# Performance work log

Hardware: AMD Instinct MI355X
Metric: run time of the kernel (lower is better)

The kernel has to match this reference:

```python
import jax, jax.numpy as jnp
import numpy as np

B_IN, C, K, P, STRIDE, ITERS = 32, 32, 3, 4, 2, 3
PSIZE = P * P


def _patch(t):
    # t: (b, h, w, B, d) -> (b, oh, ow, K, K, B, d), matching torch fancy-index patching
    b, h, w = t.shape[:3]
    oh = int((h - K + 1) / STRIDE)
    idx = (np.arange(oh) * STRIDE)[:, None] + np.arange(K)[None, :]  # (oh, K)
    t = t[:, idx]          # (b, oh, K, w, B, d)
    t = t[:, :, :, idx]    # (b, oh, K, ow, K, B, d)
    perm = (0, 1, 3, 2, 4) + tuple(range(5, t.ndim))
    return jnp.transpose(t, perm), oh, oh


def _forward(x, a, weights, beta_u, beta_a):
    b = x.shape[0]
    KKB = K * K * B_IN
    p_in, oh, ow = _patch(x)
    a_in, _, _ = _patch(a)
    pose = p_in.reshape(b, oh, ow, KKB, P, P)
    a_in = a_in.reshape(b, oh, ow, KKB, 1)
    # voting: per-capsule 4x4 matmul with transformation matrices
    v = jnp.einsum('bhwnij,ncjl->bhwncil', pose, weights).reshape(b, oh, ow, KKB, C, PSIZE)
    eps = 1e-6
    lam = 1e-3
    ln2pi = np.float32(np.log(2.0 * np.pi))
    mu = sigma_sq = a_out = None
    for it in range(ITERS):
        if it == 0:
            r = jnp.full((b, oh, ow, KKB, C), 1.0 / C, jnp.float32) * a_in  # a_in broadcasts over C
        else:
            # gaussian log-likelihood of each vote under each output capsule
            ln_pjh = -(v - mu) ** 2 / (2.0 * sigma_sq) - 0.5 * jnp.log(sigma_sq) - 0.5 * ln2pi
            ln_ap = ln_pjh.sum(axis=5) + jnp.log(a_out.reshape(b, oh, ow, 1, C))
            r = jax.nn.softmax(ln_ap, axis=4)
        r_sum = r.sum(axis=3, keepdims=True)               # (b,oh,ow,1,C)
        coeff = (r / (r_sum + eps))[..., None]             # (b,oh,ow,KKB,C,1)
        mu = (coeff * v).sum(axis=3, keepdims=True)        # (b,oh,ow,1,C,PSIZE)
        sigma_sq = (coeff * (v - mu) ** 2).sum(axis=3, keepdims=True) + eps
        # beta_u: (C,1) broadcasts against (...,C,PSIZE); log(sqrt(s)) == 0.5*log(s)
        cost_h = (beta_u + 0.5 * jnp.log(sigma_sq)) * r_sum[..., None]
        a_out = jax.nn.sigmoid(lam * (beta_a - cost_h.sum(axis=5, keepdims=True)))
    p_out = mu.reshape(b, oh, ow, C, PSIZE)
    a_out = a_out.reshape(b, oh, ow, C, 1)
    return p_out, a_out


def setup_inputs() -> dict:
    key = jax.random.key(0)
    k1, k2, k3, k4, k5 = jax.random.split(key, 5)
    x = jax.random.normal(k1, (8, 14, 14, B_IN, PSIZE), jnp.float32)
    a = jax.random.uniform(k2, (8, 14, 14, B_IN, 1), jnp.float32)
    weights = jax.random.normal(k3, (K * K * B_IN, C, P, P), jnp.float32)
    beta_u = jax.random.normal(k4, (C, 1), jnp.float32) * 0.1
    beta_a = jax.random.normal(k5, (C, 1), jnp.float32) * 0.1
    return {"x": x, "a": a, "weights": weights, "beta_u": beta_u, "beta_a": beta_a}


def reference(x, a, weights, beta_u, beta_a):
    return _forward(x, a, weights, beta_u, beta_a)
```

## Files before the change

kernel.cpp:

```cpp
#include <hip/hip_runtime.h>

#define APB 256
#define NPOS 288
#define NCH 6
#define CHUNK 48
#define PSTRIDE 1056


template<int IT>
__global__ __launch_bounds__(APB) void caps_acc(
    const float* __restrict__ xg,
    const float* __restrict__ ag,
    const float* __restrict__ wg,
    const float* __restrict__ bu,
    const float* __restrict__ ba,
    const float* __restrict__ pin,
    float* __restrict__ pout)
{
    __shared__ __align__(16) float pose_s[CHUNK * 16];
    __shared__ float a_s[CHUNK];
    __shared__ __align__(16) float scratch[4 * 32 * 33];
    __shared__ float rsum_part[4 * 32];
    __shared__ float mu_tab[512];
    __shared__ float i2s_tab[512];
    __shared__ float Kc_tab[32];

    const int tid = threadIdx.x;
    const int blk = blockIdx.x;
    const int pos = blk / NCH;
    const int ch  = blk - pos * NCH;
    const int bb  = pos / 36;
    const int rem = pos % 36;
    const int yy  = rem / 6;
    const int xx  = rem % 6;

    #pragma unroll
    for (int j = 0; j < 3; ++j) {
        const int e    = ch * 768 + j * 256 + tid;
        const int cell = e >> 9;
        const int off  = e & 511;
        const int kh = cell / 3, kw = cell % 3;
        pose_s[j * 256 + tid] =
            xg[(size_t)((((bb * 14) + (2 * yy + kh)) * 14 + (2 * xx + kw)) * 32) * 16 + off];
    }
    if (IT == 0) {
        if (tid < CHUNK) {
            const int e    = ch * CHUNK + tid;
            const int cell = e >> 5;
            const int bi   = e & 31;
            const int kh = cell / 3, kw = cell % 3;
            a_s[tid] = ag[(size_t)(((bb * 14) + (2 * yy + kh)) * 14 + (2 * xx + kw)) * 32 + bi];
        }
    }

    const int fc2 = tid >> 3;
    const int fh  = tid & 7;
    if (IT > 0) {
        const float* q0 = pin + (size_t)pos * (NCH * PSTRIDE) + fc2 * 33;
        float ms0 = 0.f, ms1 = 0.f, vs0 = 0.f, vs1 = 0.f, rsc = 0.f;
        #pragma unroll
        for (int cc = 0; cc < NCH; ++cc) {
            const float* q = q0 + cc * PSTRIDE;
            ms0 += q[fh];
            ms1 += q[fh + 8];
            vs0 += q[16 + fh];
            vs1 += q[16 + fh + 8];
            rsc += q[32];
        }
        const float inv  = 1.f / (rsc + 1e-6f);
        const float S    = rsc * inv;
        const float mu0  = ms0 * inv;
        const float mu1  = ms1 * inv;
        const float sig0 = vs0 * inv - mu0 * mu0 * (2.f - S) + 1e-6f;
        const float sig1 = vs1 * inv - mu1 * mu1 * (2.f - S) + 1e-6f;
        float lgs = __logf(sig0) + __logf(sig1);
        #pragma unroll
        for (int msk = 4; msk >= 1; msk >>= 1) lgs += __shfl_xor(lgs, msk);
        const float cost = rsc * (16.f * bu[fc2] + 0.5f * lgs);
        const float ao   = 1.f / (1.f + __expf(-0.001f * (ba[fc2] - cost)));
        mu_tab[fc2 * 16 + fh]      = mu0;
        mu_tab[fc2 * 16 + fh + 8]  = mu1;
        i2s_tab[fc2 * 16 + fh]     = 0.5f / sig0;
        i2s_tab[fc2 * 16 + fh + 8] = 0.5f / sig1;
        if (fh == 0) Kc_tab[fc2] = 0.5f * lgs - __logf(ao);
    }
    __syncthreads();

    const int c    = tid & 31;
    const int s    = tid >> 5;
    const int lane = tid & 63;
    const int wv   = tid >> 6;
    const float4* wp = (const float4*)wg;

    float mu_c[16], i2s_c[16], Kc = 0.f;
    if (IT > 0) {
        #pragma unroll
        for (int p = 0; p < 16; ++p) {
            mu_c[p]  = mu_tab[c * 16 + p];
            i2s_c[p] = i2s_tab[c * 16 + p];
        }
        Kc = Kc_tab[c];
    }
    float macc[16], vacc[16], rs = 0.f;
    #pragma unroll
    for (int p = 0; p < 16; ++p) { macc[p] = 0.f; vacc[p] = 0.f; }

    for (int k = 0; k < 6; ++k) {
        const int nl = s * 6 + k;
        const int n  = ch * CHUNK + nl;
        const float4* pp = (const float4*)&pose_s[nl << 4];
        float pf[16];
        float4 q;
        q = pp[0]; pf[0]=q.x;  pf[1]=q.y;  pf[2]=q.z;  pf[3]=q.w;
        q = pp[1]; pf[4]=q.x;  pf[5]=q.y;  pf[6]=q.z;  pf[7]=q.w;
        q = pp[2]; pf[8]=q.x;  pf[9]=q.y;  pf[10]=q.z; pf[11]=q.w;
        q = pp[3]; pf[12]=q.x; pf[13]=q.y; pf[14]=q.z; pf[15]=q.w;
        const int wbase = (n * 32 + c) * 4;
        float v[16];
        #pragma unroll
        for (int p = 0; p < 16; ++p) v[p] = 0.f;
        #pragma unroll
        for (int j = 0; j < 4; ++j) {
            const float4 w = wp[wbase + j];
            #pragma unroll
            for (int i = 0; i < 4; ++i) {
                const float pj = pf[i * 4 + j];
                v[i*4+0] = fmaf(pj, w.x, v[i*4+0]);
                v[i*4+1] = fmaf(pj, w.y, v[i*4+1]);
                v[i*4+2] = fmaf(pj, w.z, v[i*4+2]);
                v[i*4+3] = fmaf(pj, w.w, v[i*4+3]);
            }
        }
        float r;
        if (IT == 0) {
            r = a_s[nl] * 0.03125f;
        } else {
            float t0 = 0.f, t1 = 0.f, t2 = 0.f, t3 = 0.f;
            #pragma unroll
            for (int p = 0; p < 16; p += 4) {
                float d0 = v[p]   - mu_c[p];   t0 = fmaf(d0*d0, i2s_c[p],   t0);
                float d1 = v[p+1] - mu_c[p+1]; t1 = fmaf(d1*d1, i2s_c[p+1], t1);
                float d2 = v[p+2] - mu_c[p+2]; t2 = fmaf(d2*d2, i2s_c[p+2], t2);
                float d3 = v[p+3] - mu_c[p+3]; t3 = fmaf(d3*d3, i2s_c[p+3], t3);
            }
            float lnap = -((t0 + t1) + (t2 + t3)) - Kc;
            float m = lnap;
            #pragma unroll
            for (int msk = 16; msk >= 1; msk >>= 1) m = fmaxf(m, __shfl_xor(m, msk));
            float e = __expf(lnap - m);
            float sum = e;
            #pragma unroll
            for (int msk = 16; msk >= 1; msk >>= 1) sum += __shfl_xor(sum, msk);
            r = e / sum;
        }
        rs += r;
        #pragma unroll
        for (int p = 0; p < 16; ++p) {
            float rv = r * v[p];
            macc[p] += rv;
            vacc[p] = fmaf(rv, v[p], vacc[p]);
        }
    }

    #pragma unroll
    for (int p = 0; p < 16; ++p) {
        macc[p] += __shfl_xor(macc[p], 32);
        vacc[p] += __shfl_xor(vacc[p], 32);
    }
    rs += __shfl_xor(rs, 32);
    if (lane < 32) {
        const int base = (wv * 32 + lane) * 33;
        #pragma unroll
        for (int p = 0; p < 16; ++p) {
            scratch[base + p]      = macc[p];
            scratch[base + 16 + p] = vacc[p];
        }
        rsum_part[wv * 32 + lane] = rs;
    }
    __syncthreads();

    float ms0 = 0.f, ms1 = 0.f, vs0 = 0.f, vs1 = 0.f, rsc = 0.f;
    #pragma unroll
    for (int w = 0; w < 4; ++w) {
        const int base = (w * 32 + fc2) * 33;
        ms0 += scratch[base + fh];
        ms1 += scratch[base + fh + 8];
        vs0 += scratch[base + 16 + fh];
        vs1 += scratch[base + 16 + fh + 8];
        rsc += rsum_part[w * 32 + fc2];
    }
    float* po = pout + (size_t)(pos * NCH + ch) * PSTRIDE + fc2 * 33;
    po[fh]          = ms0;
    po[fh + 8]      = ms1;
    po[16 + fh]     = vs0;
    po[16 + fh + 8] = vs1;
    if (fh == 0) po[32] = rsc;
}

__global__ __launch_bounds__(512) void caps_fin(
    const float* __restrict__ pin,
    const float* __restrict__ bu,
    const float* __restrict__ ba,
    float* __restrict__ outp)
{
    const int tid = threadIdx.x;
    const int pos = blockIdx.x;
    const int fc = tid >> 4, fp = tid & 15;
    const float* q0 = pin + (size_t)pos * (NCH * PSTRIDE) + fc * 33;
    float ms = 0.f, vs = 0.f, rsc = 0.f;
    #pragma unroll
    for (int cc = 0; cc < NCH; ++cc) {
        const float* q = q0 + cc * PSTRIDE;
        ms  += q[fp];
        vs  += q[16 + fp];
        rsc += q[32];
    }
    const float inv = 1.f / (rsc + 1e-6f);
    const float S   = rsc * inv;
    const float mu  = ms * inv;
    const float sig = vs * inv - mu * mu * (2.f - S) + 1e-6f;
    const float lg  = __logf(sig);
    float lgs = lg;
    #pragma unroll
    for (int msk = 8; msk >= 1; msk >>= 1) lgs += __shfl_xor(lgs, msk);
    const float cost = rsc * (16.f * bu[fc] + 0.5f * lgs);
    const float ao   = 1.f / (1.f + __expf(-0.001f * (ba[fc] - cost)));
    outp[(size_t)pos * 512 + tid] = mu;
    if (fp == 0) outp[147456 + (size_t)pos * 32 + fc] = ao;
}

__global__ __launch_bounds__(512) void convcaps_kernel(
    const float* __restrict__ xg,
    const float* __restrict__ ag,
    const float* __restrict__ wg,
    const float* __restrict__ bu,
    const float* __restrict__ ba,
    float* __restrict__ outp)
{
    __shared__ __align__(16) float pose_s[4608];
    __shared__ float a_s[288];
    __shared__ __align__(16) float scratch[8448];
    __shared__ float rsum_part[256];
    __shared__ float mu_tab[512];
    __shared__ float i2s_tab[512];
    __shared__ float aout_tab[32];
    __shared__ float Kc_tab[32];

    const int tid = threadIdx.x;
    const int pos = blockIdx.x;
    const int bb  = pos / 36;
    const int rem = pos % 36;
    const int yy  = rem / 6;
    const int xx  = rem % 6;

    #pragma unroll
    for (int wi = 0; wi < 9; ++wi) {
        const int kh = wi / 3, kw = wi % 3;
        const float* src =
            xg + (size_t)((((bb * 14) + (2 * yy + kh)) * 14 + (2 * xx + kw)) * 32) * 16;
        pose_s[wi * 512 + tid] = src[tid];
    }
    if (tid < 288) {
        const int wi = tid >> 5, bi = tid & 31;
        const int kh = wi / 3, kw = wi % 3;
        a_s[tid] = ag[(size_t)(((bb * 14) + (2 * yy + kh)) * 14 + (2 * xx + kw)) * 32 + bi];
    }
    __syncthreads();

    const int c    = tid & 31;
    const int s    = tid >> 5;
    const int lane = tid & 63;
    const int wv   = tid >> 6;
    const float4* wp = (const float4*)wg;

    for (int it = 0; it < 3; ++it) {
        float mu_c[16], i2s_c[16], Kc = 0.f;
        if (it > 0) {
            #pragma unroll
            for (int p = 0; p < 16; ++p) {
                mu_c[p]  = mu_tab[c * 16 + p];
                i2s_c[p] = i2s_tab[c * 16 + p];
            }
            Kc = Kc_tab[c];
        }
        float macc[16], vacc[16], rs = 0.f;
        #pragma unroll
        for (int p = 0; p < 16; ++p) { macc[p] = 0.f; vacc[p] = 0.f; }

        for (int k = 0; k < 18; ++k) {
            const int n = s * 18 + k;
            const float4* pp = (const float4*)&pose_s[n << 4];
            float pf[16];
            float4 q;
            q = pp[0]; pf[0]=q.x; pf[1]=q.y; pf[2]=q.z;  pf[3]=q.w;
            q = pp[1]; pf[4]=q.x; pf[5]=q.y; pf[6]=q.z;  pf[7]=q.w;
            q = pp[2]; pf[8]=q.x; pf[9]=q.y; pf[10]=q.z; pf[11]=q.w;
            q = pp[3]; pf[12]=q.x; pf[13]=q.y; pf[14]=q.z; pf[15]=q.w;
            const int wbase = (n * 32 + c) * 4;
            float v[16];
            #pragma unroll
            for (int p = 0; p < 16; ++p) v[p] = 0.f;
            #pragma unroll
            for (int j = 0; j < 4; ++j) {
                const float4 w = wp[wbase + j];
                #pragma unroll
                for (int i = 0; i < 4; ++i) {
                    const float pj = pf[i * 4 + j];
                    v[i*4+0] = fmaf(pj, w.x, v[i*4+0]);
                    v[i*4+1] = fmaf(pj, w.y, v[i*4+1]);
                    v[i*4+2] = fmaf(pj, w.z, v[i*4+2]);
                    v[i*4+3] = fmaf(pj, w.w, v[i*4+3]);
                }
            }
            float r;
            if (it == 0) {
                r = a_s[n] * 0.03125f;
            } else {
                float t = 0.f;
                #pragma unroll
                for (int p = 0; p < 16; ++p) {
                    float d = v[p] - mu_c[p];
                    t = fmaf(d * d, i2s_c[p], t);
                }
                float lnap = -t - Kc;
                float m = lnap;
                #pragma unroll
                for (int msk = 16; msk >= 1; msk >>= 1) m = fmaxf(m, __shfl_xor(m, msk));
                float e = __expf(lnap - m);
                float sum = e;
                #pragma unroll
                for (int msk = 16; msk >= 1; msk >>= 1) sum += __shfl_xor(sum, msk);
                r = e / sum;
            }
            rs += r;
            #pragma unroll
            for (int p = 0; p < 16; ++p) {
                float rv = r * v[p];
                macc[p] += rv;
                vacc[p] = fmaf(rv, v[p], vacc[p]);
            }
        }

        #pragma unroll
        for (int p = 0; p < 16; ++p) {
            macc[p] += __shfl_xor(macc[p], 32);
            vacc[p] += __shfl_xor(vacc[p], 32);
        }
        rs += __shfl_xor(rs, 32);
        if (lane < 32) {
            const int base = (wv * 32 + lane) * 33;
            #pragma unroll
            for (int p = 0; p < 16; ++p) {
                scratch[base + p]      = macc[p];
                scratch[base + 16 + p] = vacc[p];
            }
            rsum_part[wv * 32 + lane] = rs;
        }
        __syncthreads();

        const int fc = tid >> 4, fp = tid & 15;
        float ms = 0.f, vs = 0.f, rsc = 0.f;
        #pragma unroll
        for (int w = 0; w < 8; ++w) {
            ms  += scratch[(w * 32 + fc) * 33 + fp];
            vs  += scratch[(w * 32 + fc) * 33 + 16 + fp];
            rsc += rsum_part[w * 32 + fc];
        }
        const float inv = 1.f / (rsc + 1e-6f);
        const float S   = rsc * inv;
        const float mu  = ms * inv;
        const float sig = vs * inv - mu * mu * (2.f - S) + 1e-6f;
        const float lg  = __logf(sig);
        float lgs = lg;
        #pragma unroll
        for (int msk = 8; msk >= 1; msk >>= 1) lgs += __shfl_xor(lgs, msk);
        const float buv  = bu[fc];
        const float bav  = ba[fc];
        const float cost = rsc * (16.f * buv + 0.5f * lgs);
        const float ao   = 1.f / (1.f + __expf(-0.001f * (bav - cost)));

        mu_tab[fc * 16 + fp]  = mu;
        i2s_tab[fc * 16 + fp] = 0.5f / sig;
        if (fp == 0) {
            aout_tab[fc] = ao;
            Kc_tab[fc]   = 0.5f * lgs - __logf(ao);
        }

        if (it == 2) {
            outp[(size_t)pos * 512 + tid] = mu;
            if (fp == 0) outp[147456 + (size_t)pos * 32 + fc] = ao;
        }
        __syncthreads();
    }
}

extern "C" void kernel_launch(void* const* d_in, const int* in_sizes, int n_in,
                              void* d_out, int out_size, void* d_ws, size_t ws_size,
                              hipStream_t stream) {
    (void)in_sizes; (void)n_in; (void)out_size;
    const float* x  = (const float*)d_in[0];
    const float* a  = (const float*)d_in[1];
    const float* w  = (const float*)d_in[2];
    const float* bu = (const float*)d_in[3];
    const float* ba = (const float*)d_in[4];
    float* out = (float*)d_out;

    const size_t buf_elems = (size_t)NPOS * NCH * PSTRIDE;
    if (ws_size < 2 * buf_elems * sizeof(float)) {
        convcaps_kernel<<<dim3(288), dim3(512), 0, stream>>>(x, a, w, bu, ba, out);
        return;
    }
    float* buf0 = (float*)d_ws;
    float* buf1 = buf0 + buf_elems;

    caps_acc<0><<<dim3(NPOS * NCH), dim3(APB), 0, stream>>>(x, a, w, bu, ba, nullptr, buf0);
    caps_acc<1><<<dim3(NPOS * NCH), dim3(APB), 0, stream>>>(x, a, w, bu, ba, buf0, buf1);
    caps_acc<2><<<dim3(NPOS * NCH), dim3(APB), 0, stream>>>(x, a, w, bu, ba, buf1, buf0);
    caps_fin<<<dim3(NPOS), dim3(512), 0, stream>>>(buf0, bu, ba, out);
}
```

Before: 142.5 us.

## Fuse routing iterations into one cooperative kernel with grid-wide syncs

Replaces the three per-iteration accumulation launches and the finalize launch with a single cooperative kernel. It uses grid.sync between EM routing iterations and keeps the pose chunk in shared memory across iterations. Work is also re-split into 3 chunks of 96 input capsules per position instead of 6 of 48, which halves the block count so the whole grid fits co-resident. The aim is to remove launch gaps and the repeated pose reloads. In exchange it pays for grid barrier latency, runs fewer blocks, and falls back to the old path if co-residency is not possible.

```diff
diff --git a/kernel.cpp b/kernel.cpp
--- a/kernel.cpp
+++ b/kernel.cpp
@@ -1,14 +1,239 @@
 #include <hip/hip_runtime.h>
-
-#define APB 256
+#include <hip/hip_cooperative_groups.h>
+
+namespace cg = cooperative_groups;
+
 #define NPOS 288
+#define PSTRIDE 1056
+#define CNCH 3
+#define CCHUNK 96
 #define NCH 6
 #define CHUNK 48
-#define PSTRIDE 1056
-
+
+__global__ __launch_bounds__(256) void caps_coop(
+    const float* __restrict__ xg,
+    const float* __restrict__ ag,
+    const float* __restrict__ wg,
+    const float* __restrict__ bu,
+    const float* __restrict__ ba,
+    float* __restrict__ buf0,
+    float* __restrict__ buf1,
+    float* __restrict__ outp)
+{
+    __shared__ __align__(16) float pose_s[CCHUNK * 16];
+    __shared__ float a_s[CCHUNK];
+    __shared__ __align__(16) float scratch[4 * 32 * 33];
+    __shared__ float rsum_part[4 * 32];
+    __shared__ float mu_tab[512];
+    __shared__ float i2s_tab[512];
+    __shared__ float Kc_tab[32];
+
+    cg::grid_group grid = cg::this_grid();
+
+    const int tid = threadIdx.x;
+    const int blk = blockIdx.x;
+    const int pos = blk / CNCH;
+    const int ch  = blk - pos * CNCH;
+    const int bb  = pos / 36;
+    const int rem = pos % 36;
+    const int yy  = rem / 6;
+    const int xx  = rem % 6;
+
+    #pragma unroll
+    for (int j = 0; j < 6; ++j) {
+        const int e    = j * 256 + tid;
+        const int cell = e >> 9;
+        const int off  = e & 511;
+        pose_s[e] =
+            xg[(size_t)((((bb * 14) + (2 * yy + ch)) * 14 + (2 * xx + cell)) * 32) * 16 + off];
+    }
+    if (tid < CCHUNK) {
+        const int cell = tid >> 5, bi = tid & 31;
+        a_s[tid] = ag[(size_t)(((bb * 14) + (2 * yy + ch)) * 14 + (2 * xx + cell)) * 32 + bi];
+    }
+    __syncthreads();
+
+    const int c    = tid & 31;
+    const int s    = tid >> 5;
+    const int lane = tid & 63;
+    const int wv   = tid >> 6;
+    const int fc2  = tid >> 3;
+    const int fh   = tid & 7;
+    const float4* wp = (const float4*)wg;
+
+    for (int it = 0; it < 3; ++it) {
+        const float* pin  = (it == 2) ? buf1 : buf0;
+        float*       pout = (it == 1) ? buf1 : buf0;
+
+        float mu_c[16], i2s_c[16], Kc = 0.f;
+        if (it > 0) {
+            const float* q0 = pin + (size_t)pos * (CNCH * PSTRIDE) + fc2 * 33;
+            float ms0 = 0.f, ms1 = 0.f, vs0 = 0.f, vs1 = 0.f, rsc = 0.f;
+            #pragma unroll
+            for (int cc = 0; cc < CNCH; ++cc) {
+                const float* q = q0 + cc * PSTRIDE;
+                ms0 += q[fh];
+                ms1 += q[fh + 8];
+                vs0 += q[16 + fh];
+                vs1 += q[16 + fh + 8];
+                rsc += q[32];
+            }
+            const float inv  = 1.f / (rsc + 1e-6f);
+            const float S    = rsc * inv;
+            const float mu0  = ms0 * inv;
+            const float mu1  = ms1 * inv;
+            const float sig0 = vs0 * inv - mu0 * mu0 * (2.f - S) + 1e-6f;
+            const float sig1 = vs1 * inv - mu1 * mu1 * (2.f - S) + 1e-6f;
+            float lgs = __logf(sig0) + __logf(sig1);
+            #pragma unroll
+            for (int msk = 4; msk >= 1; msk >>= 1) lgs += __shfl_xor(lgs, msk);
+            const float cost = rsc * (16.f * bu[fc2] + 0.5f * lgs);
+            const float ao   = 1.f / (1.f + __expf(-0.001f * (ba[fc2] - cost)));
+            mu_tab[fc2 * 16 + fh]      = mu0;
+            mu_tab[fc2 * 16 + fh + 8]  = mu1;
+            i2s_tab[fc2 * 16 + fh]     = 0.5f / sig0;
+            i2s_tab[fc2 * 16 + fh + 8] = 0.5f / sig1;
+            if (fh == 0) Kc_tab[fc2] = 0.5f * lgs - __logf(ao);
+            __syncthreads();
+            #pragma unroll
+            for (int p = 0; p < 16; ++p) {
+                mu_c[p]  = mu_tab[c * 16 + p];
+                i2s_c[p] = i2s_tab[c * 16 + p];
+            }
+            Kc = Kc_tab[c];
+        }
+
+        float macc[16], vacc[16], rs = 0.f;
+        #pragma unroll
+        for (int p = 0; p < 16; ++p) { macc[p] = 0.f; vacc[p] = 0.f; }
+
+        for (int k = 0; k < 12; ++k) {
+            const int nl = s * 12 + k;
+            const int n  = ch * CCHUNK + nl;
+            const float4* pp = (const float4*)&pose_s[nl << 4];
+            float pf[16];
+            float4 q;
+            q = pp[0]; pf[0]=q.x;  pf[1]=q.y;  pf[2]=q.z;  pf[3]=q.w;
+            q = pp[1]; pf[4]=q.x;  pf[5]=q.y;  pf[6]=q.z;  pf[7]=q.w;
+            q = pp[2]; pf[8]=q.x;  pf[9]=q.y;  pf[10]=q.z; pf[11]=q.w;
+            q = pp[3]; pf[12]=q.x; pf[13]=q.y; pf[14]=q.z; pf[15]=q.w;
+            const int wbase = (n * 32 + c) * 4;
+            float v[16];
+            #pragma unroll
+            for (int p = 0; p < 16; ++p) v[p] = 0.f;
+            #pragma unroll
+            for (int j = 0; j < 4; ++j) {
+                const float4 w = wp[wbase + j];
+                #pragma unroll
+                for (int i = 0; i < 4; ++i) {
+                    const float pj = pf[i * 4 + j];
+                    v[i*4+0] = fmaf(pj, w.x, v[i*4+0]);
+                    v[i*4+1] = fmaf(pj, w.y, v[i*4+1]);
+                    v[i*4+2] = fmaf(pj, w.z, v[i*4+2]);
+                    v[i*4+3] = fmaf(pj, w.w, v[i*4+3]);
+                }
+            }
+            float r;
+            if (it == 0) {
+                r = a_s[nl] * 0.03125f;
+            } else {
+                float t0 = 0.f, t1 = 0.f, t2 = 0.f, t3 = 0.f;
+                #pragma unroll
+                for (int p = 0; p < 16; p += 4) {
+                    float d0 = v[p]   - mu_c[p];   t0 = fmaf(d0*d0, i2s_c[p],   t0);
+                    float d1 = v[p+1] - mu_c[p+1]; t1 = fmaf(d1*d1, i2s_c[p+1], t1);
+                    float d2 = v[p+2] - mu_c[p+2]; t2 = fmaf(d2*d2, i2s_c[p+2], t2);
+                    float d3 = v[p+3] - mu_c[p+3]; t3 = fmaf(d3*d3, i2s_c[p+3], t3);
+                }
+                float lnap = -((t0 + t1) + (t2 + t3)) - Kc;
+                float m = lnap;
+                #pragma unroll
+                for (int msk = 16; msk >= 1; msk >>= 1) m = fmaxf(m, __shfl_xor(m, msk));
+                float e = __expf(lnap - m);
+                float sum = e;
+                #pragma unroll
+                for (int msk = 16; msk >= 1; msk >>= 1) sum += __shfl_xor(sum, msk);
+                r = e / sum;
+            }
+            rs += r;
+            #pragma unroll
+            for (int p = 0; p < 16; ++p) {
+                float rv = r * v[p];
+                macc[p] += rv;
+                vacc[p] = fmaf(rv, v[p], vacc[p]);
+            }
+        }
+
+        #pragma unroll
+        for (int p = 0; p < 16; ++p) {
+            macc[p] += __shfl_xor(macc[p], 32);
+            vacc[p] += __shfl_xor(vacc[p], 32);
+        }
+        rs += __shfl_xor(rs, 32);
+        if (lane < 32) {
+            const int base = (wv * 32 + lane) * 33;
+            #pragma unroll
+            for (int p = 0; p < 16; ++p) {
+                scratch[base + p]      = macc[p];
+                scratch[base + 16 + p] = vacc[p];
+            }
+            rsum_part[wv * 32 + lane] = rs;
+        }
+        __syncthreads();
+
+        float ms0 = 0.f, ms1 = 0.f, vs0 = 0.f, vs1 = 0.f, rsc = 0.f;
+        #pragma unroll
+        for (int w = 0; w < 4; ++w) {
+            const int base = (w * 32 + fc2) * 33;
+            ms0 += scratch[base + fh];
+            ms1 += scratch[base + fh + 8];
+            vs0 += scratch[base + 16 + fh];
+            vs1 += scratch[base + 16 + fh + 8];
+            rsc += rsum_part[w * 32 + fc2];
+        }
+        float* po = pout + (size_t)(pos * CNCH + ch) * PSTRIDE + fc2 * 33;
+        po[fh]          = ms0;
+        po[fh + 8]      = ms1;
+        po[16 + fh]     = vs0;
+        po[16 + fh + 8] = vs1;
+        if (fh == 0) po[32] = rsc;
+
+        __threadfence();
+        grid.sync();
+    }
+
+    if (ch == 0) {
+        const float* q0p = buf0 + (size_t)pos * (CNCH * PSTRIDE);
+        #pragma unroll
+        for (int half = 0; half < 2; ++half) {
+            const int fc = (tid >> 4) + half * 16;
+            const int fp = tid & 15;
+            const float* q0 = q0p + fc * 33;
+            float ms = 0.f, vs = 0.f, rsc = 0.f;
+            #pragma unroll
+            for (int cc = 0; cc < CNCH; ++cc) {
+                const float* q = q0 + cc * PSTRIDE;
+                ms  += q[fp];
+                vs  += q[16 + fp];
+                rsc += q[32];
+            }
+            const float inv = 1.f / (rsc + 1e-6f);
+            const float S   = rsc * inv;
+            const float mu  = ms * inv;
+            const float sig = vs * inv - mu * mu * (2.f - S) + 1e-6f;
+            float lgs = __logf(sig);
+            #pragma unroll
+            for (int msk = 8; msk >= 1; msk >>= 1) lgs += __shfl_xor(lgs, msk);
+            const float cost = rsc * (16.f * bu[fc] + 0.5f * lgs);
+            const float ao   = 1.f / (1.f + __expf(-0.001f * (ba[fc] - cost)));
+            outp[(size_t)pos * 512 + fc * 16 + fp] = mu;
+            if (fp == 0) outp[147456 + (size_t)pos * 32 + fc] = ao;
+        }
+    }
+}
 
 template<int IT>
-__global__ __launch_bounds__(APB) void caps_acc(
+__global__ __launch_bounds__(256) void caps_acc(
     const float* __restrict__ xg,
     const float* __restrict__ ag,
     const float* __restrict__ wg,
@@ -219,8 +444,7 @@
     const float S   = rsc * inv;
     const float mu  = ms * inv;
     const float sig = vs * inv - mu * mu * (2.f - S) + 1e-6f;
-    const float lg  = __logf(sig);
-    float lgs = lg;
+    float lgs = __logf(sig);
     #pragma unroll
     for (int msk = 8; msk >= 1; msk >>= 1) lgs += __shfl_xor(lgs, msk);
     const float cost = rsc * (16.f * bu[fc] + 0.5f * lgs);
@@ -243,7 +467,6 @@
     __shared__ float rsum_part[256];
     __shared__ float mu_tab[512];
     __shared__ float i2s_tab[512];
-    __shared__ float aout_tab[32];
     __shared__ float Kc_tab[32];
 
     const int tid = threadIdx.x;
@@ -370,21 +593,15 @@
         const float S   = rsc * inv;
         const float mu  = ms * inv;
         const float sig = vs * inv - mu * mu * (2.f - S) + 1e-6f;
-        const float lg  = __logf(sig);
-        float lgs = lg;
+        float lgs = __logf(sig);
         #pragma unroll
         for (int msk = 8; msk >= 1; msk >>= 1) lgs += __shfl_xor(lgs, msk);
-        const float buv  = bu[fc];
-        const float bav  = ba[fc];
-        const float cost = rsc * (16.f * buv + 0.5f * lgs);
-        const float ao   = 1.f / (1.f + __expf(-0.001f * (bav - cost)));
+        const float cost = rsc * (16.f * bu[fc] + 0.5f * lgs);
+        const float ao   = 1.f / (1.f + __expf(-0.001f * (ba[fc] - cost)));
 
         mu_tab[fc * 16 + fp]  = mu;
         i2s_tab[fc * 16 + fp] = 0.5f / sig;
-        if (fp == 0) {
-            aout_tab[fc] = ao;
-            Kc_tab[fc]   = 0.5f * lgs - __logf(ao);
-        }
+        if (fp == 0) Kc_tab[fc] = 0.5f * lgs - __logf(ao);
 
         if (it == 2) {
             outp[(size_t)pos * 512 + tid] = mu;
@@ -413,8 +630,32 @@
     float* buf0 = (float*)d_ws;
     float* buf1 = buf0 + buf_elems;
 
-    caps_acc<0><<<dim3(NPOS * NCH), dim3(APB), 0, stream>>>(x, a, w, bu, ba, nullptr, buf0);
-    caps_acc<1><<<dim3(NPOS * NCH), dim3(APB), 0, stream>>>(x, a, w, bu, ba, buf0, buf1);
-    caps_acc<2><<<dim3(NPOS * NCH), dim3(APB), 0, stream>>>(x, a, w, bu, ba, buf1, buf0);
+    static int coop_ok = -1;
+    if (coop_ok < 0) {
+        int dev = 0;
+        (void)hipGetDevice(&dev);
+        int coopAttr = 0, nCU = 0, nb = 0;
+        (void)hipDeviceGetAttribute(&coopAttr, hipDeviceAttributeCooperativeLaunch, dev);
+        (void)hipDeviceGetAttribute(&nCU, hipDeviceAttributeMultiprocessorCount, dev);
+        hipError_t oe = hipOccupancyMaxActiveBlocksPerMultiprocessor(&nb, caps_coop, 256, 0);
+        coop_ok = (coopAttr != 0 && oe == hipSuccess && nCU > 0 &&
+                   (long)nb * (long)nCU >= (long)(NPOS * CNCH)) ? 1 : 0;
+    }
+
+    if (coop_ok == 1) {
+        void* args[8];
+        args[0] = (void*)&x;  args[1] = (void*)&a;  args[2] = (void*)&w;
+        args[3] = (void*)&bu; args[4] = (void*)&ba;
+        args[5] = (void*)&buf0; args[6] = (void*)&buf1; args[7] = (void*)&out;
+        hipError_t e = hipLaunchCooperativeKernel((const void*)caps_coop,
+                                                  dim3(NPOS * CNCH), dim3(256),
+                                                  args, 0, stream);
+        if (e == hipSuccess) return;
+        coop_ok = 0;
+    }
+
+    caps_acc<0><<<dim3(NPOS * NCH), dim3(256), 0, stream>>>(x, a, w, bu, ba, nullptr, buf0);
+    caps_acc<1><<<dim3(NPOS * NCH), dim3(256), 0, stream>>>(x, a, w, bu, ba, buf0, buf1);
+    caps_acc<2><<<dim3(NPOS * NCH), dim3(256), 0, stream>>>(x, a, w, bu, ba, buf1, buf0);
     caps_fin<<<dim3(NPOS), dim3(512), 0, stream>>>(buf0, bu, ba, out);
 }
```

New measurement: 142.7 us. Within noise of the previous version (+0.1%).
